# Optimization experiments

Hardware: AMD Instinct MI355X
Metric: run time of the kernel (lower is better)

## Reference

```python
import jax, jax.numpy as jnp
import numpy as np

RGB_W = (0.2989, 0.587, 0.114)
EPS = 1e-8  # guard only; original divides without eps


def _saliency_map(img):
    """Faithful jax port of SaliencyMap: gray -> uint8 -> cv2.Sobel(ksize=3,
    BORDER_REFLECT_101) -> magnitude -> per-image min-max normalize.
    img: [B, C, H, W] float in [0,1]. Returns [B, 1, H, W] float32.
    """
    B, C, H, W = img.shape
    if C == 3:
        gray = RGB_W[0] * img[:, 0] + RGB_W[1] * img[:, 1] + RGB_W[2] * img[:, 2]
    else:
        gray = img[:, 0]
    # (gray*255).astype(np.uint8): truncating cast, then cv2 promotes to float
    q = (gray * 255.0).astype(jnp.uint8).astype(jnp.float32)  # [B,H,W]
    # cv2 default border: BORDER_REFLECT_101 == jnp.pad mode 'reflect'
    p = jnp.pad(q, ((0, 0), (1, 1), (1, 1)), mode='reflect')  # [B,H+2,W+2]
    # Sobel x (correlation with [[-1,0,1],[-2,0,2],[-1,0,1]])
    gx = (p[:, :-2, 2:] + 2.0 * p[:, 1:-1, 2:] + p[:, 2:, 2:]
          - p[:, :-2, :-2] - 2.0 * p[:, 1:-1, :-2] - p[:, 2:, :-2])
    # Sobel y (transpose kernel)
    gy = (p[:, 2:, :-2] + 2.0 * p[:, 2:, 1:-1] + p[:, 2:, 2:]
          - p[:, :-2, :-2] - 2.0 * p[:, :-2, 1:-1] - p[:, :-2, 2:])
    mag = jnp.sqrt(gx * gx + gy * gy)  # [B,H,W]
    mn = jnp.min(mag, axis=(1, 2), keepdims=True)
    mx = jnp.max(mag, axis=(1, 2), keepdims=True)
    norm = (mag - mn) / jnp.maximum(mx - mn, EPS)  # cv2 NORM_MINMAX to [0,1]
    return norm[:, None]  # [B,1,H,W]


def setup_inputs() -> dict:
    key = jax.random.key(0)
    k1, k2, k3 = jax.random.split(key, 3)
    shape = (16, 3, 512, 512)
    return {
        "img_vis": jax.random.uniform(k1, shape, dtype=jnp.float32),
        "img_ir": jax.random.uniform(k2, shape, dtype=jnp.float32),
        "img_fusion": jax.random.uniform(k3, shape, dtype=jnp.float32),
    }


def reference(img_vis, img_ir, img_fusion):
    s_vis = _saliency_map(img_vis)  # [B,1,H,W]
    s_ir = _saliency_map(img_ir)
    denom = s_vis + s_ir + EPS  # eps guard against 0/0 (see notes)
    w_vis = s_vis / denom
    w_ir = s_ir / denom
    img_sal = w_vis * img_vis + w_ir * img_ir  # broadcasts over channels
    loss = jnp.mean(jnp.abs(img_sal - img_fusion))  # F.l1_loss (mean)
    return loss
```

## Files before the change

### kernel.cpp

```cpp
#include <hip/hip_runtime.h>
#include <hip/hip_bf16.h>
#include <stdint.h>

#define H 512
#define W 512
#define HW (H * W)
#define TR 8
#define NSTRIP (H / TR)
#define NSLOT (TR + 2)
#define LSTR 520

__device__ __forceinline__ int refl(int i, int n) {
    return i < 0 ? -i : (i >= n ? 2 * n - 2 - i : i);
}

__device__ __forceinline__ void cols10(uint2 lo, uint2 hi, float* __restrict__ c) {
    c[0] = (float)(lo.x >> 24);
    c[1] = (float)(lo.y & 0xffu);
    c[2] = (float)((lo.y >> 8) & 0xffu);
    c[3] = (float)((lo.y >> 16) & 0xffu);
    c[4] = (float)(lo.y >> 24);
    c[5] = (float)(hi.x & 0xffu);
    c[6] = (float)((hi.x >> 8) & 0xffu);
    c[7] = (float)((hi.x >> 16) & 0xffu);
    c[8] = (float)(hi.x >> 24);
    c[9] = (float)(hi.y & 0xffu);
}

__global__ __launch_bounds__(256) void k_sal(const float* __restrict__ vis,
                                             const float* __restrict__ ir,
                                             uint8_t* __restrict__ qvis,
                                             uint8_t* __restrict__ qir,
                                             float* __restrict__ pm, int B) {
    __shared__ uint8_t g[NSLOT][LSTR];
    __shared__ float red[4][2];
    int tid = threadIdx.x;
    int per_src = B * NSTRIP;
    int blk = blockIdx.x;
    int src = blk >= per_src;
    int rem = src ? blk - per_src : blk;
    int b     = rem >> 6;
    int strip = rem & 63;
    int y0 = strip * TR;

    const float4* p4 = (const float4*)((src ? ir : vis) + (size_t)b * 3 * HW);
    uint8_t* q = (src ? qir : qvis) + (size_t)b * HW;

    float4 R[5], G[5], Bl[5];
    #pragma unroll
    for (int it = 0; it < 5; ++it) {
        int t = tid + it * 256;
        int j = t >> 7, seg = t & 127;
        int row = refl(y0 - 1 + j, H);
        int o = row * (W / 4) + seg;
        R[it]  = p4[o];
        G[it]  = p4[o + HW / 4];
        Bl[it] = p4[o + 2 * (HW / 4)];
    }
    __builtin_amdgcn_sched_barrier(0);
    #pragma unroll
    for (int it = 0; it < 5; ++it) {
        int t = tid + it * 256;
        int j = t >> 7, seg = t & 127;
        uchar4 qq;
        qq.x = (uint8_t)((0.2989f * R[it].x + 0.587f * G[it].x + 0.114f * Bl[it].x) * 255.0f);
        qq.y = (uint8_t)((0.2989f * R[it].y + 0.587f * G[it].y + 0.114f * Bl[it].y) * 255.0f);
        qq.z = (uint8_t)((0.2989f * R[it].z + 0.587f * G[it].z + 0.114f * Bl[it].z) * 255.0f);
        qq.w = (uint8_t)((0.2989f * R[it].w + 0.587f * G[it].w + 0.114f * Bl[it].w) * 255.0f);
        *(uchar4*)&g[j][4 + seg * 4] = qq;
    }
    __syncthreads();
    if (tid < NSLOT) {
        g[tid][3]   = g[tid][5];
        g[tid][516] = g[tid][514];
    }
    __syncthreads();

    float mn = INFINITY, mx = 0.0f;
    #pragma unroll
    for (int k = 0; k < 2; ++k) {
        int task = tid + k * 256;
        int r  = task >> 6;
        int s8 = task & 63;
        const uint8_t* rp0 = &g[r][s8 * 8];
        const uint8_t* rp1 = &g[r + 1][s8 * 8];
        const uint8_t* rp2 = &g[r + 2][s8 * 8];
        uint2 a0 = *(const uint2*)rp0, b0 = *(const uint2*)(rp0 + 8);
        uint2 a1 = *(const uint2*)rp1, b1 = *(const uint2*)(rp1 + 8);
        uint2 a2 = *(const uint2*)rp2, b2 = *(const uint2*)(rp2 + 8);
        uint2 qw; qw.x = a1.y; qw.y = b1.x;
        *(uint2*)(q + (size_t)(y0 + r) * W + s8 * 8) = qw;
        float c0[10], c1[10], c2[10];
        cols10(a0, b0, c0);
        cols10(a1, b1, c1);
        cols10(a2, b2, c2);
        float sx[10], sy[10];
        #pragma unroll
        for (int j = 0; j < 10; ++j) {
            sx[j] = c0[j] + 2.0f * c1[j] + c2[j];
            sy[j] = c2[j] - c0[j];
        }
        #pragma unroll
        for (int p = 0; p < 8; ++p) {
            float gx = sx[p + 2] - sx[p];
            float gy = sy[p] + 2.0f * sy[p + 1] + sy[p + 2];
            float m = sqrtf(gx * gx + gy * gy);
            mn = fminf(mn, m);
            mx = fmaxf(mx, m);
        }
    }

    #pragma unroll
    for (int o = 32; o > 0; o >>= 1) {
        mn = fminf(mn, __shfl_down(mn, o));
        mx = fmaxf(mx, __shfl_down(mx, o));
    }
    int lane = tid & 63, w = tid >> 6;
    if (lane == 0) { red[w][0] = mn; red[w][1] = mx; }
    __syncthreads();
    if (tid == 0) {
        #pragma unroll
        for (int ww = 1; ww < 4; ++ww) {
            mn = fminf(mn, red[ww][0]);
            mx = fmaxf(mx, red[ww][1]);
        }
        float* o = pm + ((size_t)(src * B + b) * NSTRIP + strip) * 2;
        o[0] = mn;
        o[1] = mx;
    }
}

__device__ __forceinline__ void row_cols(uint2 v, int lane, float* __restrict__ c) {
    uint32_t lx = __shfl_up(v.y, 1);
    uint32_t rx = __shfl_down(v.x, 1);
    uint32_t lb = (lane == 0)  ? ((v.x >> 8) & 0xffu)  : (lx >> 24);
    uint32_t rb = (lane == 63) ? ((v.y >> 16) & 0xffu) : (rx & 0xffu);
    c[0] = (float)lb;
    c[1] = (float)(v.x & 0xffu);
    c[2] = (float)((v.x >> 8) & 0xffu);
    c[3] = (float)((v.x >> 16) & 0xffu);
    c[4] = (float)(v.x >> 24);
    c[5] = (float)(v.y & 0xffu);
    c[6] = (float)((v.y >> 8) & 0xffu);
    c[7] = (float)((v.y >> 16) & 0xffu);
    c[8] = (float)(v.y >> 24);
    c[9] = (float)rb;
}

__device__ __forceinline__ void sobel_row8(const uint8_t* __restrict__ q, int y, int lane,
                                           float* __restrict__ mag) {
    const uint2* rm = (const uint2*)(q + (size_t)refl(y - 1, H) * W);
    const uint2* r0 = (const uint2*)(q + (size_t)y * W);
    const uint2* rp = (const uint2*)(q + (size_t)refl(y + 1, H) * W);
    uint2 vm = rm[lane], v0 = r0[lane], vp = rp[lane];
    float c0[10], c1[10], c2[10];
    row_cols(vm, lane, c0);
    row_cols(v0, lane, c1);
    row_cols(vp, lane, c2);
    float sx[10], sy[10];
    #pragma unroll
    for (int j = 0; j < 10; ++j) {
        sx[j] = c0[j] + 2.0f * c1[j] + c2[j];
        sy[j] = c2[j] - c0[j];
    }
    #pragma unroll
    for (int k = 0; k < 8; ++k) {
        float gx = sx[k + 2] - sx[k];
        float gy = sy[k] + 2.0f * sy[k + 1] + sy[k + 2];
        mag[k] = sqrtf(gx * gx + gy * gy);
    }
}

__global__ __launch_bounds__(256) void k_loss(const float* __restrict__ vis,
                                              const float* __restrict__ ir,
                                              const float* __restrict__ fus,
                                              const uint8_t* __restrict__ qvis,
                                              const uint8_t* __restrict__ qir,
                                              const float* __restrict__ pm,
                                              float* __restrict__ partial, int B) {
    int w = threadIdx.x >> 6, lane = threadIdx.x & 63;
    int b = blockIdx.x >> 6;
    int y0 = (blockIdx.x & 63) * 8;

    __shared__ float sred[4];
    {
        int src = w >> 1, qsel = w & 1;
        float v = pm[((size_t)(src * B + b) * NSTRIP + lane) * 2 + qsel];
        if (qsel == 0) {
            #pragma unroll
            for (int o = 32; o > 0; o >>= 1) v = fminf(v, __shfl_down(v, o));
        } else {
            #pragma unroll
            for (int o = 32; o > 0; o >>= 1) v = fmaxf(v, __shfl_down(v, o));
        }
        if (lane == 0) sred[w] = v;
    }
    __syncthreads();
    float mn_v = sred[0], mx_v = sred[1], mn_i = sred[2], mx_i = sred[3];
    float inv_v = 1.0f / fmaxf(mx_v - mn_v, 1e-8f);
    float inv_i = 1.0f / fmaxf(mx_i - mn_i, 1e-8f);

    float acc = 0.0f;
    #pragma unroll
    for (int rr = 0; rr < 2; ++rr) {
        int y = y0 + w + rr * 4;
        float mv[8], mi[8];
        sobel_row8(qvis + (size_t)b * HW, y, lane, mv);
        sobel_row8(qir  + (size_t)b * HW, y, lane, mi);

        float wv[8], wi[8];
        #pragma unroll
        for (int k = 0; k < 8; ++k) {
            float sv = (mv[k] - mn_v) * inv_v;
            float si = (mi[k] - mn_i) * inv_i;
            float den = sv + si + 1e-8f;
            float rden = 1.0f / den;
            wv[k] = sv * rden;
            wi[k] = si * rden;
        }

        int i = y * W + lane * 8;
        #pragma unroll
        for (int ch = 0; ch < 3; ++ch) {
            size_t e4 = ((((size_t)b * 3 + ch) * HW) + i) >> 2;
            const float4* v4 = (const float4*)vis;
            const float4* r4 = (const float4*)ir;
            const float4* f4 = (const float4*)fus;
            float4 va = v4[e4], vb = v4[e4 + 1];
            float4 ra = r4[e4], rb = r4[e4 + 1];
            float4 fa = f4[e4], fb = f4[e4 + 1];
            acc += fabsf(wv[0] * va.x + wi[0] * ra.x - fa.x);
            acc += fabsf(wv[1] * va.y + wi[1] * ra.y - fa.y);
            acc += fabsf(wv[2] * va.z + wi[2] * ra.z - fa.z);
            acc += fabsf(wv[3] * va.w + wi[3] * ra.w - fa.w);
            acc += fabsf(wv[4] * vb.x + wi[4] * rb.x - fb.x);
            acc += fabsf(wv[5] * vb.y + wi[5] * rb.y - fb.y);
            acc += fabsf(wv[6] * vb.z + wi[6] * rb.z - fb.z);
            acc += fabsf(wv[7] * vb.w + wi[7] * rb.w - fb.w);
        }
    }

    #pragma unroll
    for (int o = 32; o > 0; o >>= 1) acc += __shfl_down(acc, o);
    __shared__ float ssum[4];
    if (lane == 0) ssum[w] = acc;
    __syncthreads();
    if (threadIdx.x == 0) partial[blockIdx.x] = ssum[0] + ssum[1] + ssum[2] + ssum[3];
}

__global__ void k_final(const float* __restrict__ partial, int n, float* __restrict__ out,
                        long long N) {
    double s = 0.0;
    for (int i = threadIdx.x; i < n; i += 256) s += (double)partial[i];
    __shared__ double sm[256];
    sm[threadIdx.x] = s;
    __syncthreads();
    for (int k = 128; k > 0; k >>= 1) {
        if (threadIdx.x < k) sm[threadIdx.x] += sm[threadIdx.x + k];
        __syncthreads();
    }
    if (threadIdx.x == 0) out[0] = (float)(sm[0] / (double)N);
}

extern "C" void kernel_launch(void* const* d_in, const int* in_sizes, int n_in,
                              void* d_out, int out_size, void* d_ws, size_t ws_size,
                              hipStream_t stream) {
    const float* vis = (const float*)d_in[0];
    const float* ir  = (const float*)d_in[1];
    const float* fus = (const float*)d_in[2];
    int B = in_sizes[0] / (3 * HW);

    uint8_t* qvis = (uint8_t*)d_ws;
    uint8_t* qir  = qvis + (size_t)B * HW;
    float* pm      = (float*)(qir + (size_t)B * HW);
    float* partial = pm + (size_t)2 * B * NSTRIP * 2;
    float* out = (float*)d_out;

    int nblk_sal = 2 * B * NSTRIP;
    k_sal<<<nblk_sal, 256, 0, stream>>>(vis, ir, qvis, qir, pm, B);

    int nblk_loss = B * (H / 8);
    k_loss<<<nblk_loss, 256, 0, stream>>>(vis, ir, fus, qvis, qir, pm, partial, B);

    k_final<<<1, 256, 0, stream>>>(partial, nblk_loss, out, (long long)B * 3 * HW);
}
```

Before: 55.20 us.

## Rewrite saliency kernel as single-wave strips with register sliding window

Replaces the 256-thread block with shared-memory staging in the saliency pass by one 64-lane wave per 8-row strip. The wave keeps a rolling three-row grayscale window in registers and gets horizontal neighbours through lane shuffles. This removes the LDS traffic and block barriers. In exchange each block has a quarter of the threads and row loads are serialized within the wave, which reduces memory-level parallelism per block and may lower occupancy efficiency.

Measured after the change: 55.19 us. About the same (-0.0%).

```diff
diff --git a/kernel.cpp b/kernel.cpp
--- a/kernel.cpp
+++ b/kernel.cpp
@@ -5,105 +5,82 @@
 #define H 512
 #define W 512
 #define HW (H * W)
-#define TR 8
-#define NSTRIP (H / TR)
-#define NSLOT (TR + 2)
-#define LSTR 520
+#define SR 8
+#define NSTRIP (H / SR)
 
 __device__ __forceinline__ int refl(int i, int n) {
     return i < 0 ? -i : (i >= n ? 2 * n - 2 - i : i);
 }
 
-__device__ __forceinline__ void cols10(uint2 lo, uint2 hi, float* __restrict__ c) {
-    c[0] = (float)(lo.x >> 24);
-    c[1] = (float)(lo.y & 0xffu);
-    c[2] = (float)((lo.y >> 8) & 0xffu);
-    c[3] = (float)((lo.y >> 16) & 0xffu);
-    c[4] = (float)(lo.y >> 24);
-    c[5] = (float)(hi.x & 0xffu);
-    c[6] = (float)((hi.x >> 8) & 0xffu);
-    c[7] = (float)((hi.x >> 16) & 0xffu);
-    c[8] = (float)(hi.x >> 24);
-    c[9] = (float)(hi.y & 0xffu);
-}
-
-__global__ __launch_bounds__(256) void k_sal(const float* __restrict__ vis,
-                                             const float* __restrict__ ir,
-                                             uint8_t* __restrict__ qvis,
-                                             uint8_t* __restrict__ qir,
-                                             float* __restrict__ pm, int B) {
-    __shared__ uint8_t g[NSLOT][LSTR];
-    __shared__ float red[4][2];
-    int tid = threadIdx.x;
+__device__ __forceinline__ void graywin(const float4* __restrict__ p4, int y, int lane,
+                                        float* __restrict__ h) {
+    int o = refl(y, H) * (W / 4) + lane * 2;
+    float4 r0 = p4[o],                  r1 = p4[o + 1];
+    float4 g0 = p4[o + HW / 4],         g1 = p4[o + 1 + HW / 4];
+    float4 b0 = p4[o + 2 * (HW / 4)],   b1 = p4[o + 1 + 2 * (HW / 4)];
+    float g[8];
+    g[0] = (float)(uint8_t)((0.2989f * r0.x + 0.587f * g0.x + 0.114f * b0.x) * 255.0f);
+    g[1] = (float)(uint8_t)((0.2989f * r0.y + 0.587f * g0.y + 0.114f * b0.y) * 255.0f);
+    g[2] = (float)(uint8_t)((0.2989f * r0.z + 0.587f * g0.z + 0.114f * b0.z) * 255.0f);
+    g[3] = (float)(uint8_t)((0.2989f * r0.w + 0.587f * g0.w + 0.114f * b0.w) * 255.0f);
+    g[4] = (float)(uint8_t)((0.2989f * r1.x + 0.587f * g1.x + 0.114f * b1.x) * 255.0f);
+    g[5] = (float)(uint8_t)((0.2989f * r1.y + 0.587f * g1.y + 0.114f * b1.y) * 255.0f);
+    g[6] = (float)(uint8_t)((0.2989f * r1.z + 0.587f * g1.z + 0.114f * b1.z) * 255.0f);
+    g[7] = (float)(uint8_t)((0.2989f * r1.w + 0.587f * g1.w + 0.114f * b1.w) * 255.0f);
+    #pragma unroll
+    for (int j = 0; j < 8; ++j) h[j + 1] = g[j];
+    float up = __shfl_up(g[7], 1);
+    float dn = __shfl_down(g[0], 1);
+    h[0] = (lane == 0)  ? g[1] : up;
+    h[9] = (lane == 63) ? g[6] : dn;
+}
+
+__global__ __launch_bounds__(64) void k_sal(const float* __restrict__ vis,
+                                            const float* __restrict__ ir,
+                                            uint8_t* __restrict__ qvis,
+                                            uint8_t* __restrict__ qir,
+                                            float* __restrict__ pm, int B) {
+    int lane = threadIdx.x;
+    int gwave = blockIdx.x;
     int per_src = B * NSTRIP;
-    int blk = blockIdx.x;
-    int src = blk >= per_src;
-    int rem = src ? blk - per_src : blk;
+    int src = gwave >= per_src;
+    int rem = src ? gwave - per_src : gwave;
     int b     = rem >> 6;
     int strip = rem & 63;
-    int y0 = strip * TR;
+    int y0 = strip * SR;
 
     const float4* p4 = (const float4*)((src ? ir : vis) + (size_t)b * 3 * HW);
     uint8_t* q = (src ? qir : qvis) + (size_t)b * HW;
 
-    float4 R[5], G[5], Bl[5];
-    #pragma unroll
-    for (int it = 0; it < 5; ++it) {
-        int t = tid + it * 256;
-        int j = t >> 7, seg = t & 127;
-        int row = refl(y0 - 1 + j, H);
-        int o = row * (W / 4) + seg;
-        R[it]  = p4[o];
-        G[it]  = p4[o + HW / 4];
-        Bl[it] = p4[o + 2 * (HW / 4)];
-    }
-    __builtin_amdgcn_sched_barrier(0);
-    #pragma unroll
-    for (int it = 0; it < 5; ++it) {
-        int t = tid + it * 256;
-        int j = t >> 7, seg = t & 127;
-        uchar4 qq;
-        qq.x = (uint8_t)((0.2989f * R[it].x + 0.587f * G[it].x + 0.114f * Bl[it].x) * 255.0f);
-        qq.y = (uint8_t)((0.2989f * R[it].y + 0.587f * G[it].y + 0.114f * Bl[it].y) * 255.0f);
-        qq.z = (uint8_t)((0.2989f * R[it].z + 0.587f * G[it].z + 0.114f * Bl[it].z) * 255.0f);
-        qq.w = (uint8_t)((0.2989f * R[it].w + 0.587f * G[it].w + 0.114f * Bl[it].w) * 255.0f);
-        *(uchar4*)&g[j][4 + seg * 4] = qq;
-    }
-    __syncthreads();
-    if (tid < NSLOT) {
-        g[tid][3]   = g[tid][5];
-        g[tid][516] = g[tid][514];
-    }
-    __syncthreads();
+    float rw[3][10];
+    graywin(p4, y0 - 1, lane, rw[0]);
+    graywin(p4, y0,     lane, rw[1]);
 
     float mn = INFINITY, mx = 0.0f;
     #pragma unroll
-    for (int k = 0; k < 2; ++k) {
-        int task = tid + k * 256;
-        int r  = task >> 6;
-        int s8 = task & 63;
-        const uint8_t* rp0 = &g[r][s8 * 8];
-        const uint8_t* rp1 = &g[r + 1][s8 * 8];
-        const uint8_t* rp2 = &g[r + 2][s8 * 8];
-        uint2 a0 = *(const uint2*)rp0, b0 = *(const uint2*)(rp0 + 8);
-        uint2 a1 = *(const uint2*)rp1, b1 = *(const uint2*)(rp1 + 8);
-        uint2 a2 = *(const uint2*)rp2, b2 = *(const uint2*)(rp2 + 8);
-        uint2 qw; qw.x = a1.y; qw.y = b1.x;
-        *(uint2*)(q + (size_t)(y0 + r) * W + s8 * 8) = qw;
-        float c0[10], c1[10], c2[10];
-        cols10(a0, b0, c0);
-        cols10(a1, b1, c1);
-        cols10(a2, b2, c2);
+    for (int r = 0; r < SR; ++r) {
+        float* hm = rw[r % 3];
+        float* h0 = rw[(r + 1) % 3];
+        float* hp = rw[(r + 2) % 3];
+        graywin(p4, y0 + r + 1, lane, hp);
+
+        uint32_t u0 = ((uint32_t)h0[1]) | ((uint32_t)h0[2] << 8) |
+                      ((uint32_t)h0[3] << 16) | ((uint32_t)h0[4] << 24);
+        uint32_t u1 = ((uint32_t)h0[5]) | ((uint32_t)h0[6] << 8) |
+                      ((uint32_t)h0[7] << 16) | ((uint32_t)h0[8] << 24);
+        uint2 qw; qw.x = u0; qw.y = u1;
+        *(uint2*)(q + (size_t)(y0 + r) * W + lane * 8) = qw;
+
         float sx[10], sy[10];
         #pragma unroll
         for (int j = 0; j < 10; ++j) {
-            sx[j] = c0[j] + 2.0f * c1[j] + c2[j];
-            sy[j] = c2[j] - c0[j];
-        }
-        #pragma unroll
-        for (int p = 0; p < 8; ++p) {
-            float gx = sx[p + 2] - sx[p];
-            float gy = sy[p] + 2.0f * sy[p + 1] + sy[p + 2];
+            sx[j] = hm[j] + 2.0f * h0[j] + hp[j];
+            sy[j] = hp[j] - hm[j];
+        }
+        #pragma unroll
+        for (int k = 0; k < 8; ++k) {
+            float gx = sx[k + 2] - sx[k];
+            float gy = sy[k] + 2.0f * sy[k + 1] + sy[k + 2];
             float m = sqrtf(gx * gx + gy * gy);
             mn = fminf(mn, m);
             mx = fmaxf(mx, m);
@@ -115,15 +92,7 @@
         mn = fminf(mn, __shfl_down(mn, o));
         mx = fmaxf(mx, __shfl_down(mx, o));
     }
-    int lane = tid & 63, w = tid >> 6;
-    if (lane == 0) { red[w][0] = mn; red[w][1] = mx; }
-    __syncthreads();
-    if (tid == 0) {
-        #pragma unroll
-        for (int ww = 1; ww < 4; ++ww) {
-            mn = fminf(mn, red[ww][0]);
-            mx = fmaxf(mx, red[ww][1]);
-        }
+    if (lane == 0) {
         float* o = pm + ((size_t)(src * B + b) * NSTRIP + strip) * 2;
         o[0] = mn;
         o[1] = mx;
@@ -277,7 +246,7 @@
     float* out = (float*)d_out;
 
     int nblk_sal = 2 * B * NSTRIP;
-    k_sal<<<nblk_sal, 256, 0, stream>>>(vis, ir, qvis, qir, pm, B);
+    k_sal<<<nblk_sal, 64, 0, stream>>>(vis, ir, qvis, qir, pm, B);
 
     int nblk_loss = B * (H / 8);
     k_loss<<<nblk_loss, 256, 0, stream>>>(vis, ir, fus, qvis, qir, pm, partial, B);
```
